# Kernel tuning notes

Hardware: AMD Instinct MI355X
Metric: run time of the kernel (lower is better)

The kernel has to match this reference:

```python
import jax, jax.numpy as jnp
import numpy as np

B, SEQ, DIM, D, K = 32, 2048, 512, 512, 128


def _ln(x, g, b, eps=1e-5):
    m = x.mean(-1, keepdims=True)
    v = ((x - m) ** 2).mean(-1, keepdims=True)
    return (x - m) / jnp.sqrt(v + eps) * g + b


def _gelu(v):
    return jax.nn.gelu(v, approximate=False)


def _diff_topk(s, k, t):
    # s: (B, N) scores; iterative relaxed top-k (Xie & Ermon style).
    def step(carry, _):
        a = jax.nn.softmax(carry / t, axis=-1)
        carry = carry + jnp.log(jnp.clip(1.0 - a, 1e-6, 1.0))
        return carry, a
    _, Ws = jax.lax.scan(step, s, None, length=k)  # (k, B, N)
    return jnp.transpose(Ws, (1, 0, 2))            # (B, k, N)


def setup_inputs():
    key = jax.random.key(0)
    ks = jax.random.split(key, 6)
    w = lambda k_, shape: jax.random.normal(k_, shape, dtype=jnp.float32) * 0.02
    return {
        'x': jax.random.normal(ks[0], (B, SEQ, DIM), dtype=jnp.float32),
        'tau': jnp.array(0.0, dtype=jnp.float32),
        'ln1_g': jnp.ones((DIM,), jnp.float32), 'ln1_b': jnp.zeros((DIM,), jnp.float32),
        'W1': w(ks[1], (DIM, D)), 'b1': jnp.zeros((D,), jnp.float32),
        'ln2_g': jnp.ones((SEQ,), jnp.float32), 'ln2_b': jnp.zeros((SEQ,), jnp.float32),
        'W2': w(ks[2], (SEQ, SEQ)), 'b2': jnp.zeros((SEQ,), jnp.float32),
        'ln3_g': jnp.ones((D,), jnp.float32), 'ln3_b': jnp.zeros((D,), jnp.float32),
        'W3': w(ks[3], (D, D + 1)), 'b3': jnp.zeros((D + 1,), jnp.float32),
        'ln4_g': jnp.ones((D,), jnp.float32), 'ln4_b': jnp.zeros((D,), jnp.float32),
        'W4': w(ks[4], (D, DIM)), 'b4': jnp.zeros((DIM,), jnp.float32),
    }


def reference(x, tau, ln1_g, ln1_b, W1, b1, ln2_g, ln2_b, W2, b2,
              ln3_g, ln3_b, W3, b3, ln4_g, ln4_b, W4, b4):
    # tok_proj: LN(dim) -> Linear(dim, D) -> GELU
    x_tok = _gelu(_ln(x, ln1_g, ln1_b) @ W1 + b1)                  # (B, N, D)
    # ch_proj over the token axis: LN(seq) -> Linear(seq, seq) -> GELU
    xt = jnp.swapaxes(x_tok, 1, 2)                                  # (B, D, N)
    x_ch = jnp.swapaxes(_gelu(_ln(xt, ln2_g, ln2_b) @ W2 + b2), 1, 2)
    # proj -> split score | features
    h = _ln(x_tok + x_ch, ln3_g, ln3_b) @ W3 + b3                   # (B, N, D+1)
    x_score, x_proj = h[..., 0], h[..., 1:]
    t = jax.nn.sigmoid(jnp.clip(tau, -2.0, 5.0))
    Wmat = _diff_topk(x_score, K, t)                                # (B, k, N)
    Z = jnp.einsum('bkn,bnd->bkd', Wmat, x_proj)                    # soft gather
    Y = jnp.einsum('bkn,bkd->bnd', Wmat, Z)                         # soft scatter
    return _ln(x_proj + Y, ln4_g, ln4_b) @ W4 + b4                  # (B, N, dim)
```

## Files before the change

### kernel.cpp

```cpp
#include <hip/hip_runtime.h>
#include <math.h>

#define B_   32
#define SEQ_ 2048
#define DIM_ 512
#define KSEL 128

typedef _Float16 f16;
typedef _Float16 half8 __attribute__((ext_vector_type(8)));
typedef float floatx4 __attribute__((ext_vector_type(4)));

#define LSTR2 32

__device__ __forceinline__ float gelu_exact(float v) {
  return 0.5f * v * (1.0f + erff(v * 0.70710678118654752440f));
}

__global__ __launch_bounds__(256) void rowstats512(const float* __restrict__ X,
                                                   float* __restrict__ mean,
                                                   float* __restrict__ rstd) {
  int row = blockIdx.x * 4 + (threadIdx.x >> 6);
  int l = threadIdx.x & 63;
  const float4* p = (const float4*)(X + (size_t)row * 512);
  float4 v0 = p[l * 2], v1 = p[l * 2 + 1];
  float s = v0.x + v0.y + v0.z + v0.w + v1.x + v1.y + v1.z + v1.w;
  float q = v0.x*v0.x + v0.y*v0.y + v0.z*v0.z + v0.w*v0.w
          + v1.x*v1.x + v1.y*v1.y + v1.z*v1.z + v1.w*v1.w;
#pragma unroll
  for (int off = 32; off > 0; off >>= 1) {
    s += __shfl_down(s, off);
    q += __shfl_down(q, off);
  }
  if (l == 0) {
    float m = s * (1.0f / 512.0f);
    float var = q * (1.0f / 512.0f) - m * m;
    mean[row] = m;
    rstd[row] = rsqrtf(var + 1e-5f);
  }
}

__global__ __launch_bounds__(256) void rowstats512_f16(const f16* __restrict__ X,
                                                       float* __restrict__ mean,
                                                       float* __restrict__ rstd) {
  int row = blockIdx.x * 4 + (threadIdx.x >> 6);
  int l = threadIdx.x & 63;
  half8 h = *(const half8*)(X + (size_t)row * 512 + l * 8);
  float s = 0.f, q = 0.f;
#pragma unroll
  for (int i = 0; i < 8; ++i) { float v = (float)h[i]; s += v; q += v * v; }
#pragma unroll
  for (int off = 32; off > 0; off >>= 1) {
    s += __shfl_down(s, off);
    q += __shfl_down(q, off);
  }
  if (l == 0) {
    float m = s * (1.0f / 512.0f);
    float var = q * (1.0f / 512.0f) - m * m;
    mean[row] = m;
    rstd[row] = rsqrtf(var + 1e-5f);
  }
}

__global__ __launch_bounds__(512) void colstats_part(const f16* __restrict__ xtok,
                                                     float2* __restrict__ part) {
  int b = blockIdx.x >> 3, pr = blockIdx.x & 7;
  int d = threadIdx.x;
  const f16* src = xtok + ((size_t)b * SEQ_ + (size_t)pr * 256) * 512 + d;
  float s = 0.f, q = 0.f;
#pragma unroll 4
  for (int i = 0; i < 256; ++i) {
    float v = (float)src[(size_t)i * 512];
    s += v; q += v * v;
  }
  part[(size_t)blockIdx.x * 512 + d] = make_float2(s, q);
}

__global__ __launch_bounds__(256) void colstats_fin(const float2* __restrict__ part,
                                                    float* __restrict__ mean,
                                                    float* __restrict__ rstd) {
  int idx = blockIdx.x * 256 + threadIdx.x;
  int b = idx >> 9;
  float s = 0.f, q = 0.f;
#pragma unroll
  for (int p = 0; p < 8; ++p) {
    float2 v = part[((size_t)(b * 8 + p)) * 512 + (idx & 511)];
    s += v.x; q += v.y;
  }
  float m = s * (1.0f / 2048.0f);
  mean[idx] = m;
  rstd[idx] = rsqrtf(q * (1.0f / 2048.0f) - m * m + 1e-5f);
}

template <typename T>
__global__ __launch_bounds__(256) void transpose_cvt(const T* __restrict__ src,
                                                     f16* __restrict__ dst,
                                                     int R, int C, long sb, long db) {
  __shared__ float tile[32][33];
  const T* s = src + (long)blockIdx.z * sb;
  f16* d = dst + (long)blockIdx.z * db;
  int c0 = blockIdx.x * 32, r0 = blockIdx.y * 32;
  int tx = threadIdx.x, ty = threadIdx.y;
#pragma unroll
  for (int i = 0; i < 4; ++i) {
    int r = r0 + ty + i * 8, c = c0 + tx;
    if (r < R && c < C) tile[ty + i * 8][tx] = (float)s[(long)r * C + c];
  }
  __syncthreads();
#pragma unroll
  for (int i = 0; i < 4; ++i) {
    int c = c0 + ty + i * 8, r = r0 + tx;
    if (c < C && r < R) d[(long)c * R + r] = (f16)tile[tx][ty + i * 8];
  }
}

__global__ __launch_bounds__(256) void trans2_kernel(const f16* __restrict__ xtok,
    const float* __restrict__ mean2, const float* __restrict__ rstd2,
    const float* __restrict__ g2, const float* __restrict__ bl2,
    f16* __restrict__ A2) {
  __shared__ float tile[32][33];
  int b = blockIdx.z;
  const f16* src = xtok + (long)b * SEQ_ * 512;
  f16* dst = A2 + (long)b * 512 * SEQ_;
  int d0 = blockIdx.x * 32, s0 = blockIdx.y * 32;
  int tx = threadIdx.x, ty = threadIdx.y;
  float m = mean2[b * 512 + d0 + tx];
  float rs = rstd2[b * 512 + d0 + tx];
#pragma unroll
  for (int i = 0; i < 4; ++i) {
    int s = s0 + ty + i * 8;
    float v = (float)src[(long)s * 512 + d0 + tx];
    tile[ty + i * 8][tx] = (v - m) * rs * g2[s] + bl2[s];
  }
  __syncthreads();
#pragma unroll
  for (int i = 0; i < 4; ++i) {
    int d = d0 + ty + i * 8, s = s0 + tx;
    dst[(long)d * SEQ_ + s] = (f16)tile[tx][ty + i * 8];
  }
}

__device__ __forceinline__ void stage_gll(const f16* __restrict__ src, long ld,
                                          int row0, int k0, f16* S, int t) {
  int w = t >> 6, lane = t & 63;
  int r = lane >> 2, c8 = (lane & 3) * 8;
#pragma unroll
  for (int i = 0; i < 2; ++i) {
    int chunk = w * 2 + i;
    const f16* g = src + (long)(row0 + chunk * 16 + r) * ld + k0 + c8;
    f16* l = S + chunk * 16 * LSTR2;
    __builtin_amdgcn_global_load_lds(
        (const __attribute__((address_space(1))) void*)g,
        (__attribute__((address_space(3))) void*)l, 16, 0, 0);
  }
}

__device__ __forceinline__ void stage_a_ln_f32(const float* __restrict__ src, long ld,
    const float* __restrict__ mean, const float* __restrict__ rstd,
    const float* __restrict__ g, const float* __restrict__ bl,
    int row0, int k0, f16* S, int t) {
  int row = t >> 1, kc = (t & 1) * 16;
  int r = row0 + row, c = k0 + kc;
  float m = mean[r], sd = rstd[r];
  const float* p = src + (long)r * ld + c;
  float v[16], gv[16], bv[16];
#pragma unroll
  for (int i = 0; i < 4; ++i) {
    float4 q = ((const float4*)p)[i];
    v[i*4+0]=q.x; v[i*4+1]=q.y; v[i*4+2]=q.z; v[i*4+3]=q.w;
    float4 gq = ((const float4*)(g + c))[i];
    gv[i*4+0]=gq.x; gv[i*4+1]=gq.y; gv[i*4+2]=gq.z; gv[i*4+3]=gq.w;
    float4 bq = ((const float4*)(bl + c))[i];
    bv[i*4+0]=bq.x; bv[i*4+1]=bq.y; bv[i*4+2]=bq.z; bv[i*4+3]=bq.w;
  }
  half8 o0, o1;
#pragma unroll
  for (int i = 0; i < 8; ++i) {
    o0[i] = (f16)((v[i] - m) * sd * gv[i] + bv[i]);
    o1[i] = (f16)((v[i + 8] - m) * sd * gv[i + 8] + bv[i + 8]);
  }
  *(half8*)(S + row * LSTR2 + kc) = o0;
  *(half8*)(S + row * LSTR2 + kc + 8) = o1;
}

__device__ __forceinline__ void stage_a_ln_f16(const f16* __restrict__ src, long ld,
    const float* __restrict__ mean, const float* __restrict__ rstd,
    const float* __restrict__ g, const float* __restrict__ bl,
    int row0, int k0, f16* S, int t) {
  int row = t >> 1, kc = (t & 1) * 16;
  int r = row0 + row, c = k0 + kc;
  float m = mean[r], sd = rstd[r];
  const f16* p = src + (long)r * ld + c;
  half8 h0 = *(const half8*)(p);
  half8 h1 = *(const half8*)(p + 8);
  float gv[16], bv[16];
#pragma unroll
  for (int i = 0; i < 4; ++i) {
    float4 gq = ((const float4*)(g + c))[i];
    gv[i*4+0]=gq.x; gv[i*4+1]=gq.y; gv[i*4+2]=gq.z; gv[i*4+3]=gq.w;
    float4 bq = ((const float4*)(bl + c))[i];
    bv[i*4+0]=bq.x; bv[i*4+1]=bq.y; bv[i*4+2]=bq.z; bv[i*4+3]=bq.w;
  }
  half8 o0, o1;
#pragma unroll
  for (int i = 0; i < 8; ++i) {
    o0[i] = (f16)(((float)h0[i] - m) * sd * gv[i] + bv[i]);
    o1[i] = (f16)(((float)h1[i] - m) * sd * gv[i + 8] + bv[i + 8]);
  }
  *(half8*)(S + row * LSTR2 + kc) = o0;
  *(half8*)(S + row * LSTR2 + kc + 8) = o1;
}

__device__ __forceinline__ void mfma_step(const f16* As, const f16* Bs, int lane,
                                          int wr, int wc, floatx4 acc[4][4]) {
  int kc = (lane >> 4) * 8;
  int rl = lane & 15;
  half8 a[4], b[4];
#pragma unroll
  for (int mi = 0; mi < 4; ++mi)
    a[mi] = *(const half8*)(As + (wr * 64 + mi * 16 + rl) * LSTR2 + kc);
#pragma unroll
  for (int ni = 0; ni < 4; ++ni)
    b[ni] = *(const half8*)(Bs + (wc * 64 + ni * 16 + rl) * LSTR2 + kc);
#pragma unroll
  for (int mi = 0; mi < 4; ++mi)
#pragma unroll
    for (int ni = 0; ni < 4; ++ni)
      acc[mi][ni] = __builtin_amdgcn_mfma_f32_16x16x32_f16(a[mi], b[ni], acc[mi][ni], 0, 0, 0);
}

#define GEMM_PROLOG \
  __shared__ __attribute__((aligned(16))) f16 As[128 * LSTR2]; \
  __shared__ __attribute__((aligned(16))) f16 Bs[128 * LSTR2]; \
  int t = threadIdx.x; \
  int lane = t & 63, w = t >> 6, wr = w >> 1, wc = w & 1; \
  floatx4 acc[4][4]; \
  _Pragma("unroll") for (int mi = 0; mi < 4; ++mi) \
  _Pragma("unroll") for (int ni = 0; ni < 4; ++ni) acc[mi][ni] = (floatx4){0.f,0.f,0.f,0.f};

__global__ __launch_bounds__(256) void g1_kernel(const float* __restrict__ x,
    const float* __restrict__ mean, const float* __restrict__ rstd,
    const float* __restrict__ g1, const float* __restrict__ bl1,
    const f16* __restrict__ W1T, const float* __restrict__ b1,
    f16* __restrict__ xtok) {
  GEMM_PROLOG
  int m0 = blockIdx.y * 128, n0 = blockIdx.x * 128;
  for (int k0 = 0; k0 < 512; k0 += 32) {
    stage_a_ln_f32(x, 512, mean, rstd, g1, bl1, m0, k0, As, t);
    stage_gll(W1T, 512, n0, k0, Bs, t);
    __syncthreads();
    mfma_step(As, Bs, lane, wr, wc, acc);
    __syncthreads();
  }
#pragma unroll
  for (int mi = 0; mi < 4; ++mi)
#pragma unroll
    for (int ni = 0; ni < 4; ++ni) {
      int c = n0 + wc * 64 + ni * 16 + (lane & 15);
      float bias = b1[c];
      int r0 = m0 + wr * 64 + mi * 16 + (lane >> 4) * 4;
#pragma unroll
      for (int j = 0; j < 4; ++j)
        xtok[(long)(r0 + j) * 512 + c] = (f16)gelu_exact(acc[mi][ni][j] + bias);
    }
}


__device__ __forceinline__ void stage_half(const f16* __restrict__ srcbase, long ld,
                                           f16* dst, int tid) {
#pragma unroll
  for (int q = 0; q < 2; ++q) {
    int row = q * 128 + (tid >> 2);
    int slot = (tid & 3) ^ ((row >> 1) & 3);
    const f16* g = srcbase + (long)row * ld + slot * 8;
    f16* lp = dst + (long)(q * 128 + (tid >> 6) * 16) * 32;
    __builtin_amdgcn_global_load_lds(
        (const __attribute__((address_space(1))) void*)g,
        (__attribute__((address_space(3))) void*)lp, 16, 0, 0);
  }
}

__device__ __forceinline__ half8 frag32(const f16* buf, int row, int sl) {
  return *(const half8*)(buf + (long)row * 32 + ((sl ^ ((row >> 1) & 3)) << 3));
}

#define ASM_BAR()      asm volatile("s_barrier" ::: "memory")
#define ASM_WAITBAR4() asm volatile("s_waitcnt vmcnt(4)\ns_barrier" ::: "memory")

__global__ __launch_bounds__(512, 2) void g2_8p(const f16* __restrict__ W2T,
    const f16* __restrict__ A2, const float* __restrict__ b2,
    const f16* __restrict__ xtok, f16* __restrict__ xsum) {
  __shared__ __attribute__((aligned(16))) f16 Ah[2][2][256 * 32];
  __shared__ __attribute__((aligned(16))) f16 Bh[2][2][256 * 32];
  int tid = threadIdx.x;
  int l = tid & 63, w = tid >> 6;
  int wr = w >> 2, wc = w & 3;
  int rl = l & 15, sl = l >> 4;
  int b = blockIdx.z;
  int m0 = blockIdx.y * 256;
  int n0 = blockIdx.x * 256;
  const f16* Am = W2T + (long)m0 * SEQ_;
  const f16* Bm = A2 + (long)b * 512 * SEQ_ + (long)n0 * SEQ_;
  const f16* xtb = xtok + (long)b * SEQ_ * 512;
  f16* xsb = xsum + (long)b * SEQ_ * 512;

  floatx4 acc[8][4];
#pragma unroll
  for (int mf = 0; mf < 8; ++mf)
#pragma unroll
    for (int nf = 0; nf < 4; ++nf) acc[mf][nf] = (floatx4){0.f, 0.f, 0.f, 0.f};

  half8 afr[4], bfr[4];

#define STAGE(base, tile, kk, dstbuf) \
  stage_half(base + (long)((tile) & 31) * 64 + (kk) * 32, SEQ_, dstbuf, tid)

#define READ_B(d, kk) \
  _Pragma("unroll") for (int nf = 0; nf < 4; ++nf) \
    bfr[nf] = frag32(Bh[d][kk], wc * 64 + nf * 16 + rl, sl);

#define READ_A(d, kk, mb) \
  _Pragma("unroll") for (int mi = 0; mi < 4; ++mi) \
    afr[mi] = frag32(Ah[d][kk], wr * 128 + ((mb) + mi) * 16 + rl, sl);

#define MFMA16(mb) \
  __builtin_amdgcn_s_setprio(1); \
  _Pragma("unroll") for (int mi = 0; mi < 4; ++mi) \
  _Pragma("unroll") for (int nf = 0; nf < 4; ++nf) \
    acc[(mb) + mi][nf] = __builtin_amdgcn_mfma_f32_16x16x32_f16(afr[mi], bfr[nf], acc[(mb) + mi][nf], 0, 0, 0); \
  __builtin_amdgcn_s_setprio(0);

  STAGE(Am, 0, 0, Ah[0][0]); STAGE(Am, 0, 1, Ah[0][1]);
  STAGE(Bm, 0, 0, Bh[0][0]); STAGE(Bm, 0, 1, Bh[0][1]);
  STAGE(Am, 1, 0, Ah[1][0]); STAGE(Bm, 1, 0, Bh[1][0]);
  asm volatile("s_waitcnt vmcnt(0)" ::: "memory");
  __builtin_amdgcn_s_barrier();

  for (int i = 0; i < 16; ++i) {
    STAGE(Am, 2 * i + 1, 1, Ah[1][1]);
    READ_B(0, 0); READ_A(0, 0, 0);
    ASM_BAR(); MFMA16(0); ASM_BAR();
    STAGE(Bm, 2 * i + 1, 1, Bh[1][1]);
    READ_A(0, 0, 4);
    ASM_BAR(); MFMA16(4); ASM_BAR();
    STAGE(Am, 2 * i + 2, 0, Ah[0][0]);
    READ_B(0, 1); READ_A(0, 1, 0);
    ASM_BAR(); MFMA16(0); ASM_BAR();
    STAGE(Bm, 2 * i + 2, 0, Bh[0][0]);
    READ_A(0, 1, 4);
    ASM_BAR(); MFMA16(4); ASM_WAITBAR4();
    STAGE(Am, 2 * i + 2, 1, Ah[0][1]);
    READ_B(1, 0); READ_A(1, 0, 0);
    ASM_BAR(); MFMA16(0); ASM_BAR();
    STAGE(Bm, 2 * i + 2, 1, Bh[0][1]);
    READ_A(1, 0, 4);
    ASM_BAR(); MFMA16(4); ASM_BAR();
    STAGE(Am, 2 * i + 3, 0, Ah[1][0]);
    READ_B(1, 1); READ_A(1, 1, 0);
    ASM_BAR(); MFMA16(0); ASM_BAR();
    STAGE(Bm, 2 * i + 3, 0, Bh[1][0]);
    READ_A(1, 1, 4);
    ASM_BAR(); MFMA16(4); ASM_WAITBAR4();
  }

#pragma unroll
  for (int mf = 0; mf < 8; ++mf) {
    int rbase = m0 + wr * 128 + mf * 16 + sl * 4;
#pragma unroll
    for (int j = 0; j < 4; ++j) {
      int r = rbase + j;
      float bias = b2[r];
      long rowoff = (long)r * 512;
#pragma unroll
      for (int nf = 0; nf < 4; ++nf) {
        int cc = n0 + wc * 64 + nf * 16 + rl;
        float v = gelu_exact(acc[mf][nf][j] + bias);
        xsb[rowoff + cc] = (f16)((float)xtb[rowoff + cc] + v);
      }
    }
  }
#undef STAGE
#undef READ_B
#undef READ_A
#undef MFMA16
}

__global__ __launch_bounds__(256) void g3_kernel(const f16* __restrict__ xsum,
    const float* __restrict__ mean, const float* __restrict__ rstd,
    const float* __restrict__ g3, const float* __restrict__ bl3,
    const f16* __restrict__ BT , const float* __restrict__ b3,
    f16* __restrict__ xproj) {
  GEMM_PROLOG
  int m0 = blockIdx.y * 128, n0 = blockIdx.x * 128;
  for (int k0 = 0; k0 < 512; k0 += 32) {
    stage_a_ln_f16(xsum, 512, mean, rstd, g3, bl3, m0, k0, As, t);
    stage_gll(BT, 512, n0, k0, Bs, t);
    __syncthreads();
    mfma_step(As, Bs, lane, wr, wc, acc);
    __syncthreads();
  }
#pragma unroll
  for (int mi = 0; mi < 4; ++mi)
#pragma unroll
    for (int ni = 0; ni < 4; ++ni) {
      int c = n0 + wc * 64 + ni * 16 + (lane & 15);
      float bias = b3[c + 1];
      int r0 = m0 + wr * 64 + mi * 16 + (lane >> 4) * 4;
#pragma unroll
      for (int j = 0; j < 4; ++j)
        xproj[(long)(r0 + j) * 512 + c] = (f16)(acc[mi][ni][j] + bias);
    }
}

__global__ __launch_bounds__(256) void score_kernel(const f16* __restrict__ xsum,
    const float* __restrict__ mean, const float* __restrict__ rstd,
    const float* __restrict__ g3, const float* __restrict__ bl3,
    const f16* __restrict__ w3c, const float* __restrict__ b3,
    float* __restrict__ xscore) {
  int row = blockIdx.x * 4 + (threadIdx.x >> 6);
  int l = threadIdx.x & 63;
  float m = mean[row], sd = rstd[row];
  half8 h = *(const half8*)(xsum + (long)row * 512 + l * 8);
  half8 wv = *(const half8*)(w3c + l * 8);
  float acc = 0.f;
#pragma unroll
  for (int i = 0; i < 8; ++i) {
    int d = l * 8 + i;
    float v = ((float)h[i] - m) * sd * g3[d] + bl3[d];
    acc += v * (float)wv[i];
  }
#pragma unroll
  for (int off = 32; off > 0; off >>= 1) acc += __shfl_down(acc, off);
  if (l == 0) xscore[row] = acc + b3[0];
}

__global__ __launch_bounds__(256) void topk_kernel(const float* __restrict__ xscore,
                                                   const float* __restrict__ tau,
                                                   f16* __restrict__ Wm) {
  int b = blockIdx.x, t = threadIdx.x;
  __shared__ float red[4];
  float tv = fminf(fmaxf(tau[0], -2.0f), 5.0f);
  float temp = 1.0f / (1.0f + expf(-tv));
  float it = 1.0f / temp;
  float c[8];
  const float* xs = xscore + (size_t)b * SEQ_;
#pragma unroll
  for (int i = 0; i < 8; ++i) c[i] = xs[t * 8 + i];
  for (int k = 0; k < KSEL; ++k) {
    float e[8];
    float p = 0.f;
#pragma unroll
    for (int i = 0; i < 8; ++i) { e[i] = expf(c[i] * it); p += e[i]; }
#pragma unroll
    for (int off = 32; off > 0; off >>= 1) p += __shfl_down(p, off);
    if ((t & 63) == 0) red[t >> 6] = p;
    __syncthreads();
    float S = red[0] + red[1] + red[2] + red[3];
    float iS = 1.0f / S;
    float a[8];
    half8 h;
#pragma unroll
    for (int i = 0; i < 8; ++i) { a[i] = e[i] * iS; h[i] = (f16)a[i]; }
    *(half8*)(Wm + ((size_t)b * KSEL + k) * SEQ_ + t * 8) = h;
#pragma unroll
    for (int i = 0; i < 8; ++i) c[i] += logf(fmaxf(1.0f - a[i], 1e-6f));
    __syncthreads();
  }
}

__global__ __launch_bounds__(256) void gz_kernel(const f16* __restrict__ Wm,
    const f16* __restrict__ xprojT, float* __restrict__ Zpart) {
  GEMM_PROLOG
  int b = blockIdx.z, kc = blockIdx.y;
  int n0 = blockIdx.x * 128;
  const f16* A = Wm + (long)b * KSEL * SEQ_;
  const f16* BT = xprojT + (long)b * 512 * SEQ_;
  float* Zb = Zpart + ((long)b * 2 + kc) * KSEL * 512;
  int kbeg = kc * 1024, kend = kbeg + 1024;
  for (int k0 = kbeg; k0 < kend; k0 += 32) {
    stage_gll(A, SEQ_, 0, k0, As, t);
    stage_gll(BT, SEQ_, n0, k0, Bs, t);
    __syncthreads();
    mfma_step(As, Bs, lane, wr, wc, acc);
    __syncthreads();
  }
#pragma unroll
  for (int mi = 0; mi < 4; ++mi)
#pragma unroll
    for (int ni = 0; ni < 4; ++ni) {
      int c = n0 + wc * 64 + ni * 16 + (lane & 15);
      int r0 = wr * 64 + mi * 16 + (lane >> 4) * 4;
#pragma unroll
      for (int j = 0; j < 4; ++j)
        Zb[(long)(r0 + j) * 512 + c] = acc[mi][ni][j];
    }
}

__global__ __launch_bounds__(256) void ztrans_kernel(const float* __restrict__ Zpart,
                                                     f16* __restrict__ ZT) {
  __shared__ float tile[32][33];
  int b = blockIdx.z;
  int c0 = blockIdx.x * 32, r0 = blockIdx.y * 32;
  int tx = threadIdx.x, ty = threadIdx.y;
  const float* p0 = Zpart + ((long)b * 2 + 0) * KSEL * 512;
  const float* p1 = Zpart + ((long)b * 2 + 1) * KSEL * 512;
#pragma unroll
  for (int i = 0; i < 4; ++i) {
    int r = r0 + ty + i * 8, c = c0 + tx;
    tile[ty + i * 8][tx] = p0[(long)r * 512 + c] + p1[(long)r * 512 + c];
  }
  __syncthreads();
  f16* d = ZT + (long)b * 512 * KSEL;
#pragma unroll
  for (int i = 0; i < 4; ++i) {
    int c = c0 + ty + i * 8, r = r0 + tx;
    d[(long)c * KSEL + r] = (f16)tile[tx][ty + i * 8];
  }
}

__global__ __launch_bounds__(256) void gy_kernel(const f16* __restrict__ WmT,
    const f16* __restrict__ ZT, const f16* __restrict__ xproj,
    f16* __restrict__ rbuf) {
  GEMM_PROLOG
  int b = blockIdx.z;
  int m0 = blockIdx.y * 128, n0 = blockIdx.x * 128;
  const f16* A = WmT + (long)b * SEQ_ * KSEL;
  const f16* BT = ZT + (long)b * 512 * KSEL;
  const f16* xpb = xproj + (long)b * SEQ_ * 512;
  f16* rb = rbuf + (long)b * SEQ_ * 512;
  for (int k0 = 0; k0 < KSEL; k0 += 32) {
    stage_gll(A, KSEL, m0, k0, As, t);
    stage_gll(BT, KSEL, n0, k0, Bs, t);
    __syncthreads();
    mfma_step(As, Bs, lane, wr, wc, acc);
    __syncthreads();
  }
#pragma unroll
  for (int mi = 0; mi < 4; ++mi)
#pragma unroll
    for (int ni = 0; ni < 4; ++ni) {
      int c = n0 + wc * 64 + ni * 16 + (lane & 15);
      int r0 = m0 + wr * 64 + mi * 16 + (lane >> 4) * 4;
#pragma unroll
      for (int j = 0; j < 4; ++j) {
        long idx = (long)(r0 + j) * 512 + c;
        rb[idx] = (f16)((float)xpb[idx] + acc[mi][ni][j]);
      }
    }
}

__global__ __launch_bounds__(256) void g4_kernel(const f16* __restrict__ rbuf,
    const float* __restrict__ mean, const float* __restrict__ rstd,
    const float* __restrict__ g4, const float* __restrict__ bl4,
    const f16* __restrict__ W4T, const float* __restrict__ b4,
    float* __restrict__ out) {
  GEMM_PROLOG
  int m0 = blockIdx.y * 128, n0 = blockIdx.x * 128;
  for (int k0 = 0; k0 < 512; k0 += 32) {
    stage_a_ln_f16(rbuf, 512, mean, rstd, g4, bl4, m0, k0, As, t);
    stage_gll(W4T, 512, n0, k0, Bs, t);
    __syncthreads();
    mfma_step(As, Bs, lane, wr, wc, acc);
    __syncthreads();
  }
#pragma unroll
  for (int mi = 0; mi < 4; ++mi)
#pragma unroll
    for (int ni = 0; ni < 4; ++ni) {
      int c = n0 + wc * 64 + ni * 16 + (lane & 15);
      float bias = b4[c];
      int r0 = m0 + wr * 64 + mi * 16 + (lane >> 4) * 4;
#pragma unroll
      for (int j = 0; j < 4; ++j)
        out[(long)(r0 + j) * 512 + c] = acc[mi][ni][j] + bias;
    }
}

extern "C" void kernel_launch(void* const* d_in, const int* in_sizes, int n_in,
                              void* d_out, int out_size, void* d_ws, size_t ws_size,
                              hipStream_t stream) {
  const float* x    = (const float*)d_in[0];
  const float* tau  = (const float*)d_in[1];
  const float* g1   = (const float*)d_in[2];
  const float* bl1  = (const float*)d_in[3];
  const float* W1   = (const float*)d_in[4];
  const float* b1   = (const float*)d_in[5];
  const float* g2   = (const float*)d_in[6];
  const float* bl2  = (const float*)d_in[7];
  const float* W2   = (const float*)d_in[8];
  const float* b2   = (const float*)d_in[9];
  const float* g3   = (const float*)d_in[10];
  const float* bl3  = (const float*)d_in[11];
  const float* W3   = (const float*)d_in[12];
  const float* b3   = (const float*)d_in[13];
  const float* g4   = (const float*)d_in[14];
  const float* bl4  = (const float*)d_in[15];
  const float* W4   = (const float*)d_in[16];
  const float* b4   = (const float*)d_in[17];
  float* out = (float*)d_out;

  const long NTOK = (long)B_ * SEQ_;

  char* ws = (char*)d_ws;
  f16* regA   = (f16*)(ws);
  f16* regB   = (f16*)(ws + (64l << 20));
  float* Zpart = (float*)(ws + (128l << 20));
  f16* W2T    = (f16*)(ws + (144l << 20));
  f16* W1T    = (f16*)(ws + (152l << 20));
  f16* W3T    = (f16*)(ws + (153l << 20));
  f16* W4T    = (f16*)(ws + (154l << 20));
  float* xscore = (float*)(ws + (155l << 20));
  float* meanA  = (float*)(ws + (156l << 20));
  float* rstdA  = meanA + NTOK;
  float* mean2  = rstdA + NTOK;
  float* rstd2  = mean2 + B_ * 512;
  float2* part  = (float2*)(rstd2 + B_ * 512);
  f16* ZT     = (f16*)(ws + (157l << 20));

  f16* xtok   = (f16*)d_out;
  f16* xprojT = (f16*)d_out;
  f16* Wm     = (f16*)((char*)d_out + (64l << 20));
  f16* WmT    = (f16*)((char*)d_out + (80l << 20));

  f16* A2    = regA;
  f16* xsum  = regB;
  f16* xproj = regA;
  f16* rbuf  = regB;

  dim3 tb(32, 8);

  transpose_cvt<float><<<dim3(16, 16, 1), tb, 0, stream>>>(W1, W1T, 512, 512, 0, 0);
  transpose_cvt<float><<<dim3(64, 64, 1), tb, 0, stream>>>(W2, W2T, 2048, 2048, 0, 0);
  transpose_cvt<float><<<dim3(17, 16, 1), tb, 0, stream>>>(W3, W3T, 512, 513, 0, 0);
  transpose_cvt<float><<<dim3(16, 16, 1), tb, 0, stream>>>(W4, W4T, 512, 512, 0, 0);

  rowstats512<<<NTOK / 4, 256, 0, stream>>>(x, meanA, rstdA);
  g1_kernel<<<dim3(4, 512), 256, 0, stream>>>(x, meanA, rstdA, g1, bl1, W1T, b1, xtok);

  colstats_part<<<B_ * 8, 512, 0, stream>>>(xtok, part);
  colstats_fin<<<64, 256, 0, stream>>>(part, mean2, rstd2);
  trans2_kernel<<<dim3(16, 64, B_), tb, 0, stream>>>(xtok, mean2, rstd2, g2, bl2, A2);
  g2_8p<<<dim3(2, 8, B_), 512, 0, stream>>>(W2T, A2, b2, xtok, xsum);

  rowstats512_f16<<<NTOK / 4, 256, 0, stream>>>(xsum, meanA, rstdA);
  score_kernel<<<NTOK / 4, 256, 0, stream>>>(xsum, meanA, rstdA, g3, bl3, W3T, b3, xscore);
  g3_kernel<<<dim3(4, 512), 256, 0, stream>>>(xsum, meanA, rstdA, g3, bl3, W3T + 512, b3, xproj);

  topk_kernel<<<B_, 256, 0, stream>>>(xscore, tau, Wm);

  transpose_cvt<f16><<<dim3(16, 64, B_), tb, 0, stream>>>(xproj, xprojT, 2048, 512,
      (long)SEQ_ * 512, (long)512 * SEQ_);
  transpose_cvt<f16><<<dim3(64, 4, B_), tb, 0, stream>>>(Wm, WmT, 128, 2048,
      (long)KSEL * SEQ_, (long)SEQ_ * KSEL);

  gz_kernel<<<dim3(4, 2, B_), 256, 0, stream>>>(Wm, xprojT, Zpart);
  ztrans_kernel<<<dim3(16, 4, B_), tb, 0, stream>>>(Zpart, ZT);

  gy_kernel<<<dim3(4, 16, B_), 256, 0, stream>>>(WmT, ZT, xproj, rbuf);

  rowstats512_f16<<<NTOK / 4, 256, 0, stream>>>(rbuf, meanA, rstdA);
  g4_kernel<<<dim3(4, 512), 256, 0, stream>>>(rbuf, meanA, rstdA, g4, bl4, W4T, b4, out);
}
```

Measured before the change: 893.7 us.

## Fuse xproj transpose into g3 epilogue and widen topk to 512 threads

```diff
diff --git a/kernel.cpp b/kernel.cpp
--- a/kernel.cpp
+++ b/kernel.cpp
@@ -8,6 +8,7 @@
 
 typedef _Float16 f16;
 typedef _Float16 half8 __attribute__((ext_vector_type(8)));
+typedef _Float16 half4 __attribute__((ext_vector_type(4)));
 typedef float floatx4 __attribute__((ext_vector_type(4)));
 
 #define LSTR2 32
@@ -283,8 +284,9 @@
   return *(const half8*)(buf + (long)row * 32 + ((sl ^ ((row >> 1) & 3)) << 3));
 }
 
-#define ASM_BAR()      asm volatile("s_barrier" ::: "memory")
-#define ASM_WAITBAR4() asm volatile("s_waitcnt vmcnt(4)\ns_barrier" ::: "memory")
+#define BAR() __builtin_amdgcn_s_barrier()
+#define WAITBAR4() do { asm volatile("s_waitcnt vmcnt(4)" ::: "memory"); \
+                        __builtin_amdgcn_s_barrier(); } while (0)
 
 __global__ __launch_bounds__(512, 2) void g2_8p(const f16* __restrict__ W2T,
     const f16* __restrict__ A2, const float* __restrict__ b2,
@@ -338,28 +340,28 @@
   for (int i = 0; i < 16; ++i) {
     STAGE(Am, 2 * i + 1, 1, Ah[1][1]);
     READ_B(0, 0); READ_A(0, 0, 0);
-    ASM_BAR(); MFMA16(0); ASM_BAR();
+    BAR(); MFMA16(0); BAR();
     STAGE(Bm, 2 * i + 1, 1, Bh[1][1]);
     READ_A(0, 0, 4);
-    ASM_BAR(); MFMA16(4); ASM_BAR();
+    BAR(); MFMA16(4); BAR();
     STAGE(Am, 2 * i + 2, 0, Ah[0][0]);
     READ_B(0, 1); READ_A(0, 1, 0);
-    ASM_BAR(); MFMA16(0); ASM_BAR();
+    BAR(); MFMA16(0); BAR();
     STAGE(Bm, 2 * i + 2, 0, Bh[0][0]);
     READ_A(0, 1, 4);
-    ASM_BAR(); MFMA16(4); ASM_WAITBAR4();
+    BAR(); MFMA16(4); WAITBAR4();
     STAGE(Am, 2 * i + 2, 1, Ah[0][1]);
     READ_B(1, 0); READ_A(1, 0, 0);
-    ASM_BAR(); MFMA16(0); ASM_BAR();
+    BAR(); MFMA16(0); BAR();
     STAGE(Bm, 2 * i + 2, 1, Bh[0][1]);
     READ_A(1, 0, 4);
-    ASM_BAR(); MFMA16(4); ASM_BAR();
+    BAR(); MFMA16(4); BAR();
     STAGE(Am, 2 * i + 3, 0, Ah[1][0]);
     READ_B(1, 1); READ_A(1, 1, 0);
-    ASM_BAR(); MFMA16(0); ASM_BAR();
+    BAR(); MFMA16(0); BAR();
     STAGE(Bm, 2 * i + 3, 0, Bh[1][0]);
     READ_A(1, 1, 4);
-    ASM_BAR(); MFMA16(4); ASM_WAITBAR4();
+    BAR(); MFMA16(4); WAITBAR4();
   }
 
 #pragma unroll
@@ -388,7 +390,7 @@
     const float* __restrict__ mean, const float* __restrict__ rstd,
     const float* __restrict__ g3, const float* __restrict__ bl3,
     const f16* __restrict__ BT , const float* __restrict__ b3,
-    f16* __restrict__ xproj) {
+    f16* __restrict__ xproj, f16* __restrict__ xprojT) {
   GEMM_PROLOG
   int m0 = blockIdx.y * 128, n0 = blockIdx.x * 128;
   for (int k0 = 0; k0 < 512; k0 += 32) {
@@ -405,9 +407,16 @@
       int c = n0 + wc * 64 + ni * 16 + (lane & 15);
       float bias = b3[c + 1];
       int r0 = m0 + wr * 64 + mi * 16 + (lane >> 4) * 4;
-#pragma unroll
-      for (int j = 0; j < 4; ++j)
-        xproj[(long)(r0 + j) * 512 + c] = (f16)(acc[mi][ni][j] + bias);
+      half4 xp;
+#pragma unroll
+      for (int j = 0; j < 4; ++j) {
+        f16 v = (f16)(acc[mi][ni][j] + bias);
+        xproj[(long)(r0 + j) * 512 + c] = v;
+        xp[j] = v;
+      }
+      long bb = r0 >> 11;
+      long rloc = r0 & 2047;
+      *(half4*)(xprojT + (bb * 512 + c) * SEQ_ + rloc) = xp;
     }
 }
 
@@ -433,37 +442,41 @@
   if (l == 0) xscore[row] = acc + b3[0];
 }
 
-__global__ __launch_bounds__(256) void topk_kernel(const float* __restrict__ xscore,
+__global__ __launch_bounds__(512) void topk_kernel(const float* __restrict__ xscore,
                                                    const float* __restrict__ tau,
                                                    f16* __restrict__ Wm) {
   int b = blockIdx.x, t = threadIdx.x;
-  __shared__ float red[4];
+  __shared__ float red[2][8];
   float tv = fminf(fmaxf(tau[0], -2.0f), 5.0f);
   float temp = 1.0f / (1.0f + expf(-tv));
   float it = 1.0f / temp;
-  float c[8];
+  float c[4];
   const float* xs = xscore + (size_t)b * SEQ_;
-#pragma unroll
-  for (int i = 0; i < 8; ++i) c[i] = xs[t * 8 + i];
+  {
+    float4 v = *(const float4*)(xs + t * 4);
+    c[0] = v.x; c[1] = v.y; c[2] = v.z; c[3] = v.w;
+  }
+  int l = t & 63, wid = t >> 6;
   for (int k = 0; k < KSEL; ++k) {
-    float e[8];
+    float e[4];
     float p = 0.f;
 #pragma unroll
-    for (int i = 0; i < 8; ++i) { e[i] = expf(c[i] * it); p += e[i]; }
+    for (int i = 0; i < 4; ++i) { e[i] = expf(c[i] * it); p += e[i]; }
 #pragma unroll
     for (int off = 32; off > 0; off >>= 1) p += __shfl_down(p, off);
-    if ((t & 63) == 0) red[t >> 6] = p;
-    __syncthreads();
-    float S = red[0] + red[1] + red[2] + red[3];
+    if (l == 0) red[k & 1][wid] = p;
+    __syncthreads();
+    float S = 0.f;
+#pragma unroll
+    for (int q = 0; q < 8; ++q) S += red[k & 1][q];
     float iS = 1.0f / S;
-    float a[8];
-    half8 h;
-#pragma unroll
-    for (int i = 0; i < 8; ++i) { a[i] = e[i] * iS; h[i] = (f16)a[i]; }
-    *(half8*)(Wm + ((size_t)b * KSEL + k) * SEQ_ + t * 8) = h;
-#pragma unroll
-    for (int i = 0; i < 8; ++i) c[i] += logf(fmaxf(1.0f - a[i], 1e-6f));
-    __syncthreads();
+    half4 h;
+    float a[4];
+#pragma unroll
+    for (int i = 0; i < 4; ++i) { a[i] = e[i] * iS; h[i] = (f16)a[i]; }
+    *(half4*)(Wm + ((size_t)b * KSEL + k) * SEQ_ + t * 4) = h;
+#pragma unroll
+    for (int i = 0; i < 4; ++i) c[i] += logf(fmaxf(1.0f - a[i], 1e-6f));
   }
 }
 
@@ -643,12 +656,11 @@
 
   rowstats512_f16<<<NTOK / 4, 256, 0, stream>>>(xsum, meanA, rstdA);
   score_kernel<<<NTOK / 4, 256, 0, stream>>>(xsum, meanA, rstdA, g3, bl3, W3T, b3, xscore);
-  g3_kernel<<<dim3(4, 512), 256, 0, stream>>>(xsum, meanA, rstdA, g3, bl3, W3T + 512, b3, xproj);
-
-  topk_kernel<<<B_, 256, 0, stream>>>(xscore, tau, Wm);
-
-  transpose_cvt<f16><<<dim3(16, 64, B_), tb, 0, stream>>>(xproj, xprojT, 2048, 512,
-      (long)SEQ_ * 512, (long)512 * SEQ_);
+  g3_kernel<<<dim3(4, 512), 256, 0, stream>>>(xsum, meanA, rstdA, g3, bl3, W3T + 512, b3,
+                                              xproj, xprojT);
+
+  topk_kernel<<<B_, 512, 0, stream>>>(xscore, tau, Wm);
+
   transpose_cvt<f16><<<dim3(64, 4, B_), tb, 0, stream>>>(Wm, WmT, 128, 2048,
       (long)KSEL * SEQ_, (long)SEQ_ * KSEL);
 
```

Result: no change. 876.2 us (-2.0%).
